# Optimization experiments

Measured on AMD Instinct MI355X. Metric: run time of the kernel, lower is better.

Reference implementation:

```python
import jax, jax.numpy as jnp
import numpy as np

B, A, G, D, H = 512, 32, 4, 1024, 16
DK = D // H            # 64
INNER = DK * H         # 1024 (== d_model since d_k defaulted)
P = A * G + 1          # 129 (with CLS token)


def _xavier(k, fout, fin):
    lim = np.sqrt(6.0 / (fin + fout)).astype(np.float32)
    return jax.random.uniform(k, (fout, fin), jnp.float32, -lim, lim)


def setup_inputs() -> dict:
    key = jax.random.key(0)
    ks = jax.random.split(key, 16)
    inp = {"x": jax.random.normal(ks[0], (B, P, D), jnp.float32)}
    names = ["q_ant", "k_ant", "v_ant", "q_freq", "k_freq", "v_freq"]
    for i, n in enumerate(names):
        inp["w_" + n] = _xavier(ks[1 + 2 * i], INNER, D if "ant" in n else INNER)
        inp["b_" + n] = jnp.zeros((INNER,), jnp.float32)
    inp["w_out"] = _xavier(ks[13], D, INNER)
    inp["b_out"] = jnp.zeros((D,), jnp.float32)
    return inp


def _sdpa(q, k, v):
    # q,k,v: [N, H, S, DK]
    scale = 1.0 / np.sqrt(DK).astype(np.float32)
    s = jnp.einsum('nhqd,nhkd->nhqk', q, k) * scale
    p = jax.nn.softmax(s, axis=-1)
    return jnp.einsum('nhqk,nhkd->nhqd', p, v)


def _heads(x, w, b, S):
    # x: [N, S, F] -> [N, H, S, DK]
    y = x @ w.T + b
    return y.reshape(-1, S, H, DK).transpose(0, 2, 1, 3)


def reference(x, w_q_ant, b_q_ant, w_k_ant, b_k_ant, w_v_ant, b_v_ant,
              w_q_freq, b_q_freq, w_k_freq, b_k_freq, w_v_freq, b_v_freq,
              w_out, b_out):
    Bv, Pv, Dv = x.shape
    cls_token = x[:, :1, :]                       # [B,1,D]
    grid = x[:, 1:, :].reshape(Bv, A, G, Dv)
    # ---- antenna-axis attention: batch over (B, freq_group) ----
    x_ant = grid.transpose(0, 2, 1, 3).reshape(Bv * G, A, Dv)
    q = _heads(x_ant, w_q_ant, b_q_ant, A)
    k = _heads(x_ant, w_k_ant, b_k_ant, A)
    v = _heads(x_ant, w_v_ant, b_v_ant, A)
    out_ant = _sdpa(q, k, v).transpose(0, 2, 1, 3).reshape(Bv * G, A, INNER)
    # ---- frequency-axis attention: batch over (B, antenna) ----
    x_freq = out_ant.reshape(Bv, G, A, INNER).transpose(0, 2, 1, 3).reshape(Bv * A, G, INNER)
    q = _heads(x_freq, w_q_freq, b_q_freq, G)
    k = _heads(x_freq, w_k_freq, b_k_freq, G)
    v = _heads(x_freq, w_v_freq, b_v_freq, G)
    out_freq = _sdpa(q, k, v).transpose(0, 2, 1, 3).reshape(Bv * A, G, INNER)
    # ---- output projection + CLS recombination (dropout=0 at eval) ----
    grid_flat = out_freq.reshape(Bv, A * G, INNER)
    grid_final = grid_flat @ w_out.T + b_out      # [B, A*G, D]
    grid_mean = grid_final.mean(axis=1, keepdims=True)
    cls_out = cls_token + grid_mean               # [B,1,D]
    grid_final = grid_final + cls_out
    return jnp.concatenate([cls_out, grid_final], axis=1)  # [B, P, D]
```

## Files before the change

### kernel.cpp

```cpp
#include <hip/hip_runtime.h>

typedef __attribute__((ext_vector_type(8))) short short8;
typedef __attribute__((ext_vector_type(4))) float f32x4;

#define DEV __device__ __forceinline__

DEV unsigned short f2bf(float f) {
  union { float f; unsigned u; } x; x.f = f;
  unsigned r = x.u + 0x7FFFu + ((x.u >> 16) & 1u);
  return (unsigned short)(r >> 16);
}
DEV float bf2f(short h) {
  union { unsigned u; float f; } x; x.u = ((unsigned)(unsigned short)h) << 16;
  return x.f;
}

DEV void gload16(const void* g, void* l) {
  __builtin_amdgcn_global_load_lds(
      (const __attribute__((address_space(1))) unsigned int*)g,
      (__attribute__((address_space(3))) unsigned int*)l, 16, 0, 0);
}

#define BARRIER() do { asm volatile("" ::: "memory"); \
  __builtin_amdgcn_s_barrier(); asm volatile("" ::: "memory"); } while (0)
#define WAIT_LGKM0() asm volatile("s_waitcnt lgkmcnt(0)" ::: "memory")
#define WAIT_VM8() asm volatile("s_waitcnt vmcnt(8)" ::: "memory")
#define WAIT_VM3() asm volatile("s_waitcnt vmcnt(3)" ::: "memory")
#define WAIT_VM0() asm volatile("s_waitcnt vmcnt(0)" ::: "memory")

struct CvtW { const float* s[7]; short* d[7]; };
__global__ __launch_bounds__(256) void cvt_weights(CvtW a) {
  int i = (blockIdx.x * 256 + threadIdx.x) * 8;
  int r = i >> 10, cix = i & 1023;
  int hh = r >> 6, dd = r & 63;
  #pragma unroll
  for (int m = 0; m < 7; ++m) {
    const float* s = a.s[m] + i;
    float4 v0 = *(const float4*)(s);
    float4 v1 = *(const float4*)(s + 4);
    short8 o;
    o[0] = (short)f2bf(v0.x); o[1] = (short)f2bf(v0.y);
    o[2] = (short)f2bf(v0.z); o[3] = (short)f2bf(v0.w);
    o[4] = (short)f2bf(v1.x); o[5] = (short)f2bf(v1.y);
    o[6] = (short)f2bf(v1.z); o[7] = (short)f2bf(v1.w);
    int dr = (m < 6) ? (hh * 192 + (m % 3) * 64 + dd) : r;
    *(short8*)(a.d[m] + (size_t)dr * 1024 + cix) = o;
  }
}

struct CvtB { const float* s[6]; float* d0; float* d1; };
__global__ __launch_bounds__(256) void cvt_bias(CvtB a) {
  int m = blockIdx.x;
  const float* s = a.s[m];
  float* dst = (m < 3) ? a.d0 : a.d1;
  int j = threadIdx.x * 4;
  int hh = j >> 6, dd = j & 63;
  float4 v = *(const float4*)(s + j);
  *(float4*)(dst + hh * 192 + (m % 3) * 64 + dd) = v;
}

__global__ __launch_bounds__(256) void permute_x(const float* __restrict__ x,
                                                 short* __restrict__ xa) {
  int m = blockIdx.x * 2 + (threadIdx.x >> 7);
  int a = m & 31, n = m >> 5;
  int g = n & 3, b = n >> 2;
  int c = (threadIdx.x & 127) * 8;
  size_t src = ((size_t)b * 129 + 1 + (size_t)a * 4 + g) * 1024 + c;
  float4 v0 = *(const float4*)(x + src);
  float4 v1 = *(const float4*)(x + src + 4);
  short8 o;
  o[0] = (short)f2bf(v0.x); o[1] = (short)f2bf(v0.y);
  o[2] = (short)f2bf(v0.z); o[3] = (short)f2bf(v0.w);
  o[4] = (short)f2bf(v1.x); o[5] = (short)f2bf(v1.y);
  o[6] = (short)f2bf(v1.z); o[7] = (short)f2bf(v1.w);
  *(short8*)(xa + (size_t)m * 1024 + c) = o;
}

#define PH_MFMA3(q) do { \
  __builtin_amdgcn_s_setprio(1); \
  _Pragma("unroll") for (int kk = 0; kk < 2; ++kk) \
    _Pragma("unroll") for (int nf = 0; nf < 3; ++nf) \
      acc[q][nf] = __builtin_amdgcn_mfma_f32_16x16x32_bf16( \
          af[kk], bf3[nf][kk], acc[q][nf], 0, 0, 0); \
  __builtin_amdgcn_s_setprio(0); } while (0)

#define LOAD_A16(q) do { \
  const char* pa = base + wm * 8192 + ((q)*16 + l15) * 128; \
  af[0] = *(const short8*)(pa + swz0); \
  af[1] = *(const short8*)(pa + swz1); \
} while (0)

template <int STAGE>
__global__ __launch_bounds__(1024)
void gemm_attn(const short* __restrict__ A, const short* __restrict__ Bm,
               const float* __restrict__ bias, short* __restrict__ Outp, int K) {
  extern __shared__ char ls[];
  int nwg = gridDim.x;
  int bid = blockIdx.x;
  bid = (bid & 7) * (nwg >> 3) + (bid >> 3);
  int tm = (bid >> 4) << 8;
  int hh = bid & 15;
  int t = threadIdx.x;
  int lane = t & 63, w = t >> 6;
  int wm = w >> 2, wn = w & 3;
  int l15 = lane & 15, l4 = lane >> 4;
  int cg = (lane & 7) ^ ((lane >> 3) & 7);

  const short* aS[2];
  #pragma unroll
  for (int s = 0; s < 2; ++s) {
    int r = (w + s * 16) * 8 + (lane >> 3);
    aS[s] = A + (size_t)(tm + r) * K + cg * 8;
  }
  const short* bS0 = Bm + (size_t)(hh * 192 + w * 8 + (lane >> 3)) * K + cg * 8;
  const short* bS1 = Bm + (size_t)(hh * 192 + ((w & 7) + 16) * 8 + (lane >> 3)) * K + cg * 8;

  auto stageA = [&](int c, int kt) {
    gload16(aS[0] + kt * 64, ls + c * 65536 + w * 1024);
    gload16(aS[1] + kt * 64, ls + c * 65536 + (w + 16) * 1024);
  };
  auto stageB = [&](int c, int kt) {
    gload16(bS0 + kt * 64, ls + c * 65536 + 32768 + w * 1024);
    if (w < 8) gload16(bS1 + kt * 64, ls + c * 65536 + 32768 + (16 + w) * 1024);
  };
  int swz0 = ((l4 ^ (l15 & 7)) << 4);
  int swz1 = swz0 ^ 64;

  f32x4 acc[4][3];
  #pragma unroll
  for (int m = 0; m < 4; ++m)
    #pragma unroll
    for (int n = 0; n < 3; ++n) acc[m][n] = (f32x4){0.f, 0.f, 0.f, 0.f};

  int NT = K >> 6;
  stageB(0, 0); stageA(0, 0);
  stageB(1, 1); stageA(1, 1);
  WAIT_VM3();
  BARRIER();

  for (int kt = 0; kt < NT; ++kt) {
    int c = kt & 1;
    const char* base = ls + c * 65536;
    bool stg = (kt + 2) < NT;
    short8 bf3[3][2], af[2];
    #pragma unroll
    for (int nf = 0; nf < 3; ++nf) {
      const char* p = base + 32768 + (wn * 48 + nf * 16 + l15) * 128;
      bf3[nf][0] = *(const short8*)(p + swz0);
      bf3[nf][1] = *(const short8*)(p + swz1);
    }
    LOAD_A16(0);
    BARRIER();
    PH_MFMA3(0);
    BARRIER();
    if (stg) stageB(c, kt + 2);
    LOAD_A16(1);
    BARRIER();
    PH_MFMA3(1);
    BARRIER();
    LOAD_A16(2);
    BARRIER();
    PH_MFMA3(2);
    BARRIER();
    LOAD_A16(3);
    WAIT_LGKM0();
    BARRIER();
    if (stg) stageA(c, kt + 2);
    PH_MFMA3(3);
    if (stg) { WAIT_VM3(); } else { WAIT_VM0(); }
    BARRIER();
  }

  const float* bb = bias + hh * 192;
  #pragma unroll
  for (int nf = 0; nf < 3; ++nf) {
    int col = wn * 48 + nf * 16 + l15;
    float bv = bb[col];
    #pragma unroll
    for (int mf = 0; mf < 4; ++mf)
      #pragma unroll
      for (int j = 0; j < 4; ++j) {
        int row = wm * 64 + mf * 16 + l4 * 4 + j;
        *(short*)(ls + row * 400 + col * 2) = (short)f2bf(acc[mf][nf][j] + bv);
      }
  }
  WAIT_LGKM0();
  BARRIER();

  if constexpr (STAGE == 1) {
    if (w < 8) {
      const char* qk = ls + (size_t)(w * 32) * 400;
      short8 qf[2][2], kf[2][2];
      #pragma unroll
      for (int mt = 0; mt < 2; ++mt)
        #pragma unroll
        for (int kk = 0; kk < 2; ++kk) {
          int row = mt * 16 + l15;
          qf[mt][kk] = *(const short8*)(qk + row * 400 + (kk * 32 + l4 * 8) * 2);
          kf[mt][kk] = *(const short8*)(qk + row * 400 + 128 + (kk * 32 + l4 * 8) * 2);
        }
      f32x4 sf[2][2];
      #pragma unroll
      for (int mt = 0; mt < 2; ++mt)
        #pragma unroll
        for (int nt = 0; nt < 2; ++nt) sf[mt][nt] = (f32x4){0.f, 0.f, 0.f, 0.f};
      #pragma unroll
      for (int kk = 0; kk < 2; ++kk)
        #pragma unroll
        for (int mt = 0; mt < 2; ++mt)
          #pragma unroll
          for (int nt = 0; nt < 2; ++nt)
            sf[mt][nt] = __builtin_amdgcn_mfma_f32_16x16x32_bf16(qf[mt][kk], kf[nt][kk], sf[mt][nt], 0, 0, 0);

      short* Pw = (short*)(ls + 102400 + w * 2560);
      #pragma unroll
      for (int mt = 0; mt < 2; ++mt)
        #pragma unroll
        for (int j = 0; j < 4; ++j) {
          float a0 = sf[mt][0][j] * 0.125f;
          float a1 = sf[mt][1][j] * 0.125f;
          float mx = fmaxf(a0, a1);
          mx = fmaxf(mx, __shfl_xor(mx, 1));
          mx = fmaxf(mx, __shfl_xor(mx, 2));
          mx = fmaxf(mx, __shfl_xor(mx, 4));
          mx = fmaxf(mx, __shfl_xor(mx, 8));
          float e0 = __expf(a0 - mx), e1 = __expf(a1 - mx);
          float sm = e0 + e1;
          sm += __shfl_xor(sm, 1);
          sm += __shfl_xor(sm, 2);
          sm += __shfl_xor(sm, 4);
          sm += __shfl_xor(sm, 8);
          float inv = 1.0f / sm;
          int row = mt * 16 + l4 * 4 + j;
          Pw[row * 40 + l15]      = (short)f2bf(e0 * inv);
          Pw[row * 40 + 16 + l15] = (short)f2bf(e1 * inv);
        }
      WAIT_LGKM0();

      short8 pa[2], vb[4];
      pa[0] = *(const short8*)(Pw + l15 * 40 + l4 * 8);
      pa[1] = *(const short8*)(Pw + (16 + l15) * 40 + l4 * 8);
      #pragma unroll
      for (int nt = 0; nt < 4; ++nt) {
        short8 v;
        #pragma unroll
        for (int j = 0; j < 8; ++j)
          v[j] = *(const short*)(qk + (l4 * 8 + j) * 400 + 256 + (nt * 16 + l15) * 2);
        vb[nt] = v;
      }
      f32x4 of[2][4];
      #pragma unroll
      for (int mt = 0; mt < 2; ++mt)
        #pragma unroll
        for (int nt = 0; nt < 4; ++nt) of[mt][nt] = (f32x4){0.f, 0.f, 0.f, 0.f};
      #pragma unroll
      for (int mt = 0; mt < 2; ++mt)
        #pragma unroll
        for (int nt = 0; nt < 4; ++nt)
          of[mt][nt] = __builtin_amdgcn_mfma_f32_16x16x32_bf16(pa[mt], vb[nt], of[mt][nt], 0, 0, 0);

      int nn = (tm >> 5) + w;
      int b = nn >> 2, g = nn & 3;
      #pragma unroll
      for (int mt = 0; mt < 2; ++mt)
        #pragma unroll
        for (int j = 0; j < 4; ++j) {
          int q = mt * 16 + l4 * 4 + j;
          size_t orow = (((size_t)b * 32 + q) * 4 + g) * 1024 + hh * 64;
          #pragma unroll
          for (int nt = 0; nt < 4; ++nt)
            Outp[orow + nt * 16 + l15] = (short)f2bf(of[mt][nt][j]);
        }
    }
  } else {
    if (t < 512) {
      int gi = t >> 3, s = t & 7, gq = s >> 1, dh = s & 1;
      const char* grp = ls + (size_t)(gi * 4) * 400;
      short8 q8[4];
      #pragma unroll
      for (int c = 0; c < 4; ++c)
        q8[c] = *(const short8*)(grp + gq * 400 + dh * 64 + c * 16);
      float dot[4];
      #pragma unroll
      for (int k = 0; k < 4; ++k) {
        float p = 0.f;
        #pragma unroll
        for (int c = 0; c < 4; ++c) {
          short8 k8 = *(const short8*)(grp + k * 400 + 128 + dh * 64 + c * 16);
          #pragma unroll
          for (int j = 0; j < 8; ++j) p += bf2f(q8[c][j]) * bf2f(k8[j]);
        }
        p += __shfl_xor(p, 1);
        dot[k] = p * 0.125f;
      }
      float mx = fmaxf(fmaxf(dot[0], dot[1]), fmaxf(dot[2], dot[3]));
      float e[4], sm = 0.f;
      #pragma unroll
      for (int k = 0; k < 4; ++k) { e[k] = __expf(dot[k] - mx); sm += e[k]; }
      float inv = 1.0f / sm;
      float o[32];
      #pragma unroll
      for (int j = 0; j < 32; ++j) o[j] = 0.f;
      #pragma unroll
      for (int k = 0; k < 4; ++k) {
        float pk = e[k] * inv;
        #pragma unroll
        for (int c = 0; c < 4; ++c) {
          short8 v8 = *(const short8*)(grp + k * 400 + 256 + dh * 64 + c * 16);
          #pragma unroll
          for (int j = 0; j < 8; ++j) o[c * 8 + j] += pk * bf2f(v8[j]);
        }
      }
      int n4 = ((tm >> 2) + gi) * 4 + gq;
      short* orow = Outp + (size_t)n4 * 1024 + hh * 64 + dh * 32;
      #pragma unroll
      for (int c = 0; c < 4; ++c) {
        short8 a8;
        #pragma unroll
        for (int j = 0; j < 8; ++j) a8[j] = (short)f2bf(o[c * 8 + j]);
        *(short8*)(orow + c * 8) = a8;
      }
    }
  }
}

#define PH_MFMA(q) do { \
  __builtin_amdgcn_s_setprio(1); \
  _Pragma("unroll") for (int kk = 0; kk < 2; ++kk) \
    _Pragma("unroll") for (int m = 0; m < 2; ++m) \
      _Pragma("unroll") for (int nf = 0; nf < 4; ++nf) \
        acc[(q)*2+m][nf] = __builtin_amdgcn_mfma_f32_16x16x32_bf16( \
            af[m][kk], bf[nf][kk], acc[(q)*2+m][nf], 0, 0, 0); \
  __builtin_amdgcn_s_setprio(0); } while (0)

#define LOAD_A(q) do { \
  const char* pa = base + aRdBase + ((q)*32 + l15) * 128; \
  af[0][0] = *(const short8*)(pa + swz0); \
  af[0][1] = *(const short8*)(pa + swz1); \
  af[1][0] = *(const short8*)(pa + 2048 + swz0); \
  af[1][1] = *(const short8*)(pa + 2048 + swz1); \
} while (0)

__global__ __launch_bounds__(512, 2)
void gemm_out(const short* __restrict__ A, const short* __restrict__ Bm,
              const float* __restrict__ bias, const float* __restrict__ x,
              float* __restrict__ Out, int M, int N, int K) {
  extern __shared__ char ls[];
  int nbn = N >> 8;
  int nwg = gridDim.x;
  int bid = blockIdx.x;
  bid = (bid & 7) * (nwg >> 3) + (bid >> 3);
  int tm = (bid / nbn) << 8;
  int tn = (bid % nbn) << 8;
  int t = threadIdx.x;
  int lane = t & 63, w = t >> 6;
  int wm = w >> 2, wn = w & 3;
  int l15 = lane & 15, l4 = lane >> 4;
  int cg = (lane & 7) ^ ((lane >> 3) & 7);
  const short* aS[2][2];
  const short* bS[2][2];
  #pragma unroll
  for (int h = 0; h < 2; ++h)
    #pragma unroll
    for (int i = 0; i < 2; ++i) {
      int r = h * 128 + (w * 2 + i) * 8 + (lane >> 3);
      aS[h][i] = A + (size_t)(tm + r) * K + cg * 8;
      bS[h][i] = Bm + (size_t)(tn + r) * K + cg * 8;
    }
  int dstOff = (w * 2) * 1024;
  auto stageA = [&](int c, int kt) {
    #pragma unroll
    for (int h = 0; h < 2; ++h)
      #pragma unroll
      for (int i = 0; i < 2; ++i)
        gload16(aS[h][i] + kt * 64, ls + c * 65536 + h * 16384 + dstOff + i * 1024);
  };
  auto stageB = [&](int c, int kt, int h) {
    #pragma unroll
    for (int i = 0; i < 2; ++i)
      gload16(bS[h][i] + kt * 64, ls + c * 65536 + 32768 + h * 16384 + dstOff + i * 1024);
  };
  int aRdBase = wm * 16384;
  int bRdBase = 32768 + (wn >> 1) * 16384;
  int bRow0 = (wn & 1) * 64;
  int swz0 = ((l4 ^ (l15 & 7)) << 4);
  int swz1 = swz0 ^ 64;
  f32x4 acc[8][4];
  #pragma unroll
  for (int m = 0; m < 8; ++m)
    #pragma unroll
    for (int n = 0; n < 4; ++n) acc[m][n] = (f32x4){0.f, 0.f, 0.f, 0.f};
  int NT = K >> 6;
  stageB(0, 0, 0); stageB(0, 0, 1); stageA(0, 0);
  stageB(1, 1, 0); stageB(1, 1, 1); stageA(1, 1);
  WAIT_VM8();
  BARRIER();
  for (int kt = 0; kt < NT; ++kt) {
    int c = kt & 1;
    const char* base = ls + c * 65536;
    bool stg = (kt + 2) < NT;
    short8 bf[4][2], af[2][2];
    #pragma unroll
    for (int nf = 0; nf < 4; ++nf) {
      const char* p = base + bRdBase + (bRow0 + nf * 16 + l15) * 128;
      bf[nf][0] = *(const short8*)(p + swz0);
      bf[nf][1] = *(const short8*)(p + swz1);
    }
    LOAD_A(0);
    BARRIER();
    PH_MFMA(0);
    BARRIER();
    if (stg) stageB(c, kt + 2, 0);
    LOAD_A(1);
    BARRIER();
    PH_MFMA(1);
    BARRIER();
    if (stg) stageB(c, kt + 2, 1);
    LOAD_A(2);
    BARRIER();
    PH_MFMA(2);
    BARRIER();
    LOAD_A(3);
    WAIT_LGKM0();
    BARRIER();
    if (stg) stageA(c, kt + 2);
    PH_MFMA(3);
    if (stg) { WAIT_VM8(); } else { WAIT_VM0(); }
    BARRIER();
  }
  int b = (tm >> 7) + wm;
  #pragma unroll
  for (int nf = 0; nf < 4; ++nf) {
    int colg = tn + wn * 64 + nf * 16 + l15;
    float bv = bias[colg];
    float s = 0.f;
    #pragma unroll
    for (int mf = 0; mf < 8; ++mf)
      #pragma unroll
      for (int j = 0; j < 4; ++j) s += acc[mf][nf][j];
    s += 32.0f * bv;
    s += __shfl_xor(s, 16);
    s += __shfl_xor(s, 32);
    float cls = x[(size_t)b * 129 * 1024 + colg] + s * (1.0f / 128.0f);
    if (l4 == 0)
      Out[((size_t)b * 129) * 1024 + colg] = cls;
    #pragma unroll
    for (int mf = 0; mf < 8; ++mf) {
      #pragma unroll
      for (int j = 0; j < 4; ++j) {
        int tok = mf * 16 + l4 * 4 + j;
        Out[((size_t)b * 129 + 1 + tok) * 1024 + colg] = acc[mf][nf][j] + bv + cls;
      }
    }
  }
}

extern "C" void kernel_launch(void* const* d_in, const int* in_sizes, int n_in,
                              void* d_out, int out_size, void* d_ws, size_t ws_size,
                              hipStream_t stream) {
  const float* x        = (const float*)d_in[0];
  const float* w_q_ant  = (const float*)d_in[1];
  const float* b_q_ant  = (const float*)d_in[2];
  const float* w_k_ant  = (const float*)d_in[3];
  const float* b_k_ant  = (const float*)d_in[4];
  const float* w_v_ant  = (const float*)d_in[5];
  const float* b_v_ant  = (const float*)d_in[6];
  const float* w_q_freq = (const float*)d_in[7];
  const float* b_q_freq = (const float*)d_in[8];
  const float* w_k_freq = (const float*)d_in[9];
  const float* b_k_freq = (const float*)d_in[10];
  const float* w_v_freq = (const float*)d_in[11];
  const float* b_v_freq = (const float*)d_in[12];
  const float* w_out    = (const float*)d_in[13];
  const float* b_out    = (const float*)d_in[14];

  char* ws = (char*)d_ws;
  size_t off = 0;
  auto carve = [&](size_t bytes) {
    char* p = ws + off;
    off += (bytes + 255) & ~(size_t)255;
    return p;
  };
  short* wcat_ant  = (short*)carve((size_t)3072 * 1024 * 2);
  short* wcat_freq = (short*)carve((size_t)3072 * 1024 * 2);
  short* wout_bf   = (short*)carve((size_t)1024 * 1024 * 2);
  float* bcat_ant  = (float*)carve(3072 * 4);
  float* bcat_freq = (float*)carve(3072 * 4);
  short* bufA = (short*)carve((size_t)65536 * 1024 * 2);
  short* bufF = (short*)carve((size_t)65536 * 1024 * 2);
  short* bufG = (short*)carve((size_t)65536 * 1024 * 2);
  (void)ws_size; (void)in_sizes; (void)n_in; (void)out_size;

  hipFuncSetAttribute((const void*)gemm_attn<1>,
                      hipFuncAttributeMaxDynamicSharedMemorySize, 131072);
  hipFuncSetAttribute((const void*)gemm_attn<2>,
                      hipFuncAttributeMaxDynamicSharedMemorySize, 131072);
  hipFuncSetAttribute((const void*)gemm_out,
                      hipFuncAttributeMaxDynamicSharedMemorySize, 131072);

  CvtW cw;
  cw.s[0] = w_q_ant;  cw.s[1] = w_k_ant;  cw.s[2] = w_v_ant;
  cw.s[3] = w_q_freq; cw.s[4] = w_k_freq; cw.s[5] = w_v_freq;
  cw.s[6] = w_out;
  cw.d[0] = wcat_ant;  cw.d[1] = wcat_ant;  cw.d[2] = wcat_ant;
  cw.d[3] = wcat_freq; cw.d[4] = wcat_freq; cw.d[5] = wcat_freq;
  cw.d[6] = wout_bf;
  cvt_weights<<<512, 256, 0, stream>>>(cw);

  CvtB cb;
  cb.s[0] = b_q_ant;  cb.s[1] = b_k_ant;  cb.s[2] = b_v_ant;
  cb.s[3] = b_q_freq; cb.s[4] = b_k_freq; cb.s[5] = b_v_freq;
  cb.d0 = bcat_ant; cb.d1 = bcat_freq;
  cvt_bias<<<6, 256, 0, stream>>>(cb);

  permute_x<<<32768, 256, 0, stream>>>(x, bufA);

  gemm_attn<1><<<4096, 1024, 131072, stream>>>(bufA, wcat_ant, bcat_ant, bufF, 1024);
  gemm_attn<2><<<4096, 1024, 131072, stream>>>(bufF, wcat_freq, bcat_freq, bufG, 1024);
  gemm_out<<<1024, 512, 131072, stream>>>(bufG, wout_bf, b_out, x, (float*)d_out,
                                          65536, 1024, 1024);
}
```

Baseline: 1.220 ms.

## Remove intra-iteration barriers and software-pipeline A-fragment LDS loads with MFMAs

The GEMM main loop used to hold a workgroup barrier between every A-fragment LDS load and each MFMA group. It now loads the four A fragments into separate registers ahead of time, interleaves them with the MFMA groups, and issues both the A and B global-to-LDS prefetches after a single barrier at the end of the iteration. The vmcnt wait becomes per-wave (4 or 3) to match the number of outstanding loads per wave. The goal is to cut barrier stalls and let LDS reads overlap MFMA work. The cost is more VGPR pressure and later issue of the prefetches, which leaves less time to hide global latency.

```diff
diff --git a/kernel.cpp b/kernel.cpp
--- a/kernel.cpp
+++ b/kernel.cpp
@@ -25,8 +25,11 @@
   __builtin_amdgcn_s_barrier(); asm volatile("" ::: "memory"); } while (0)
 #define WAIT_LGKM0() asm volatile("s_waitcnt lgkmcnt(0)" ::: "memory")
 #define WAIT_VM8() asm volatile("s_waitcnt vmcnt(8)" ::: "memory")
-#define WAIT_VM3() asm volatile("s_waitcnt vmcnt(3)" ::: "memory")
 #define WAIT_VM0() asm volatile("s_waitcnt vmcnt(0)" ::: "memory")
+#define WAIT_VM_TILE() do { if (w < 8) { \
+    asm volatile("s_waitcnt vmcnt(4)" ::: "memory"); \
+  } else { \
+    asm volatile("s_waitcnt vmcnt(3)" ::: "memory"); } } while (0)
 
 struct CvtW { const float* s[7]; short* d[7]; };
 __global__ __launch_bounds__(256) void cvt_weights(CvtW a) {
@@ -76,18 +79,18 @@
   *(short8*)(xa + (size_t)m * 1024 + c) = o;
 }
 
-#define PH_MFMA3(q) do { \
+#define MFMA_GRP(q, AF) do { \
   __builtin_amdgcn_s_setprio(1); \
   _Pragma("unroll") for (int kk = 0; kk < 2; ++kk) \
     _Pragma("unroll") for (int nf = 0; nf < 3; ++nf) \
       acc[q][nf] = __builtin_amdgcn_mfma_f32_16x16x32_bf16( \
-          af[kk], bf3[nf][kk], acc[q][nf], 0, 0, 0); \
+          AF[kk], bf3[nf][kk], acc[q][nf], 0, 0, 0); \
   __builtin_amdgcn_s_setprio(0); } while (0)
 
-#define LOAD_A16(q) do { \
+#define LOAD_A16(DST, q) do { \
   const char* pa = base + wm * 8192 + ((q)*16 + l15) * 128; \
-  af[0] = *(const short8*)(pa + swz0); \
-  af[1] = *(const short8*)(pa + swz1); \
+  DST[0] = *(const short8*)(pa + swz0); \
+  DST[1] = *(const short8*)(pa + swz1); \
 } while (0)
 
 template <int STAGE>
@@ -135,39 +138,32 @@
   int NT = K >> 6;
   stageB(0, 0); stageA(0, 0);
   stageB(1, 1); stageA(1, 1);
-  WAIT_VM3();
+  WAIT_VM_TILE();
   BARRIER();
 
   for (int kt = 0; kt < NT; ++kt) {
     int c = kt & 1;
     const char* base = ls + c * 65536;
     bool stg = (kt + 2) < NT;
-    short8 bf3[3][2], af[2];
+    short8 bf3[3][2], afA[2], afB[2], afC[2], afD[2];
     #pragma unroll
     for (int nf = 0; nf < 3; ++nf) {
       const char* p = base + 32768 + (wn * 48 + nf * 16 + l15) * 128;
       bf3[nf][0] = *(const short8*)(p + swz0);
       bf3[nf][1] = *(const short8*)(p + swz1);
     }
-    LOAD_A16(0);
-    BARRIER();
-    PH_MFMA3(0);
-    BARRIER();
-    if (stg) stageB(c, kt + 2);
-    LOAD_A16(1);
-    BARRIER();
-    PH_MFMA3(1);
-    BARRIER();
-    LOAD_A16(2);
-    BARRIER();
-    PH_MFMA3(2);
-    BARRIER();
-    LOAD_A16(3);
+    LOAD_A16(afA, 0);
+    LOAD_A16(afB, 1);
+    MFMA_GRP(0, afA);
+    LOAD_A16(afC, 2);
+    MFMA_GRP(1, afB);
+    LOAD_A16(afD, 3);
+    MFMA_GRP(2, afC);
+    MFMA_GRP(3, afD);
     WAIT_LGKM0();
     BARRIER();
-    if (stg) stageA(c, kt + 2);
-    PH_MFMA3(3);
-    if (stg) { WAIT_VM3(); } else { WAIT_VM0(); }
+    if (stg) { stageA(c, kt + 2); stageB(c, kt + 2); }
+    if (stg) { WAIT_VM_TILE(); } else { WAIT_VM0(); }
     BARRIER();
   }
 
```

Result: slower. 1.274 ms (+4.4%).
